# Performance work log

Hardware: AMD Instinct MI355X
Metric: run time of the kernel (lower is better)

Reference implementation:

```python
import jax, jax.numpy as jnp
import numpy as np

N = 50000   # nodes
E = 500000  # edges
NEG_SLOPE = 0.2


def _edge_softmax(e, dst, n):
    # softmax over edges grouped by destination node (DGL edge_softmax)
    m = jax.ops.segment_max(e, dst, num_segments=n)          # [N,H]
    ex = jnp.exp(e - m[dst])
    s = jax.ops.segment_sum(ex, dst, num_segments=n)
    return ex / s[dst]


def _gat(h, W, al, ar, b, src, dst, heads, d, Wres=None, act=True):
    # DGL GATConv (eval mode, no dropout)
    n = h.shape[0]
    feat = (h @ W).reshape(n, heads, d)                      # [N,H,D]
    el = jnp.sum(feat * al[None], axis=-1)                   # [N,H]
    er = jnp.sum(feat * ar[None], axis=-1)                   # [N,H]
    e = jax.nn.leaky_relu(el[src] + er[dst], NEG_SLOPE)      # [E,H]
    a = _edge_softmax(e, dst, n)                             # [E,H]
    rst = jax.ops.segment_sum(feat[src] * a[..., None], dst, num_segments=n)  # [N,H,D]
    if Wres is not None:
        res = (h @ Wres).reshape(n, heads, d)
    else:
        res = h.reshape(n, heads, d)                         # identity residual (in == heads*d)
    rst = rst + res + b.reshape(1, heads, d)
    if act:
        rst = jax.nn.elu(rst)
    return rst.reshape(n, heads * d)


def _bn(x, g, b, m, v):
    # BatchNorm1d in eval mode
    return (x - m) * g * jax.lax.rsqrt(v + 1e-5) + b


def setup_inputs() -> dict:
    key = jax.random.key(0)
    ks = jax.random.split(key, 40)
    rn = lambda i, s: jax.random.normal(ks[i], s, jnp.float32) * 0.1
    inp = dict(
        node_feats=jax.random.normal(ks[0], (N, 128), jnp.float32),
        edge_feats=jax.random.normal(ks[1], (E, 64), jnp.float32),
        src=jax.random.randint(ks[2], (E,), 0, N, jnp.int32),
        dst=jax.random.randint(ks[3], (E,), 0, N, jnp.int32),
        # GAT layer 0: 128 -> 8 heads x 16
        W0=rn(4, (128, 128)), al0=rn(5, (8, 16)), ar0=rn(6, (8, 16)), b0=rn(7, (128,)),
        g0=1.0 + rn(8, (128,)), bt0=rn(9, (128,)), m0=rn(10, (128,)),
        v0=1.0 + 0.1 * jax.random.uniform(ks[11], (128,), jnp.float32),
        # GAT layer 1: 128 -> 8 heads x 8 (residual projection)
        W1=rn(12, (128, 64)), al1=rn(13, (8, 8)), ar1=rn(14, (8, 8)), b1=rn(15, (64,)),
        Wres1=rn(16, (128, 64)),
        g1=1.0 + rn(17, (64,)), bt1=rn(18, (64,)), m1=rn(19, (64,)),
        v1=1.0 + 0.1 * jax.random.uniform(ks[20], (64,), jnp.float32),
        # GAT layer 2: 64 -> 1 head x 32 (residual projection, no activation)
        W2=rn(21, (64, 32)), al2=rn(22, (1, 32)), ar2=rn(23, (1, 32)), b2=rn(24, (32,)),
        Wres2=rn(25, (64, 32)),
        g2=1.0 + rn(26, (32,)), bt2=rn(27, (32,)), m2=rn(28, (32,)),
        v2=1.0 + 0.1 * jax.random.uniform(ks[29], (32,), jnp.float32),
        # edge projection 64 -> 128
        We=rn(30, (64, 128)), be=rn(31, (128,)),
        # edge classifier: 192 -> 32 -> 16 -> 2
        Wc1=rn(32, (192, 32)), bc1=rn(33, (32,)),
        Wc2=rn(34, (32, 16)), bc2=rn(35, (16,)),
        Wc3=rn(36, (16, 2)), bc3=rn(37, (2,)),
    )
    return inp


def reference(node_feats, edge_feats, src, dst,
              W0, al0, ar0, b0, g0, bt0, m0, v0,
              W1, al1, ar1, b1, Wres1, g1, bt1, m1, v1,
              W2, al2, ar2, b2, Wres2, g2, bt2, m2, v2,
              We, be, Wc1, bc1, Wc2, bc2, Wc3, bc3):
    h = _bn(_gat(node_feats, W0, al0, ar0, b0, src, dst, 8, 16), g0, bt0, m0, v0)
    h = _bn(_gat(h, W1, al1, ar1, b1, src, dst, 8, 8, Wres1), g1, bt1, m1, v1)
    h = _bn(_gat(h, W2, al2, ar2, b2, src, dst, 1, 32, Wres2, act=False), g2, bt2, m2, v2)
    ef = jax.nn.relu(edge_feats @ We + be)                   # [E,128]
    rep = jnp.concatenate([h[src], h[dst], ef], axis=1)      # [E,192]
    z = jax.nn.relu(rep @ Wc1 + bc1)
    z = jax.nn.relu(z @ Wc2 + bc2)
    return z @ Wc3 + bc3                                     # [E,2]
```

## Files before the change

### kernel.cpp

```cpp
#include <hip/hip_runtime.h>
#include <cfloat>
#include <math.h>

#define NEG_SLOPE 0.2f

typedef short short8 __attribute__((ext_vector_type(8)));
typedef float f32x4 __attribute__((ext_vector_type(4)));

__device__ __forceinline__ short f2bf(float x) {
    unsigned u = __float_as_uint(x);
    u += 0x7fffu + ((u >> 16) & 1u);
    return (short)(u >> 16);
}
__device__ __forceinline__ float bf2f(unsigned short s) {
    return __uint_as_float((unsigned)s << 16);
}

__device__ __forceinline__ void lds_fence() {
    __asm__ __volatile__("s_waitcnt lgkmcnt(0)" ::: "memory");
}


__global__ void count_deg_k(const int* __restrict__ dst, int* __restrict__ deg, int E) {
    int i = blockIdx.x * 256 + threadIdx.x;
    if (i < E) atomicAdd(&deg[dst[i]], 1);
}

__global__ void scanA_k(const int* __restrict__ deg, int* __restrict__ csum, int n) {
    int t = blockIdx.x * 256 + threadIdx.x;
    int ch = (n + 4095) >> 12;
    int beg = t * ch, end = min(beg + ch, n);
    int s = 0;
    for (int i = beg; i < end; ++i) s += deg[i];
    csum[t] = s;
}

__global__ void scanB_k(int* __restrict__ csum) {
    __shared__ int part[1024];
    int tid = threadIdx.x;
    int c[4];
    int s = 0;
#pragma unroll
    for (int i = 0; i < 4; ++i) { c[i] = csum[tid * 4 + i]; s += c[i]; }
    part[tid] = s;
    __syncthreads();
    for (int d = 1; d < 1024; d <<= 1) {
        int v = (tid >= d) ? part[tid - d] : 0;
        __syncthreads();
        part[tid] += v;
        __syncthreads();
    }
    int base = (tid > 0) ? part[tid - 1] : 0;
#pragma unroll
    for (int i = 0; i < 4; ++i) { csum[tid * 4 + i] = base; base += c[i]; }
}

__global__ void scanC_k(const int* __restrict__ deg, const int* __restrict__ csum,
                        int* __restrict__ off, int n, int E) {
    int t = blockIdx.x * 256 + threadIdx.x;
    int ch = (n + 4095) >> 12;
    int beg = t * ch, end = min(beg + ch, n);
    int run = csum[t];
    for (int i = beg; i < end; ++i) { off[i] = run; run += deg[i]; }
    if (t == 0) off[n] = E;
}

__global__ void scatter_k(const int* __restrict__ src, const int* __restrict__ dst,
                          const int* __restrict__ off, int* __restrict__ cur,
                          int* __restrict__ srcp, int E) {
    int i = blockIdx.x * 256 + threadIdx.x;
    if (i >= E) return;
    int d = dst[i];
    int p = off[d] + atomicAdd(&cur[d], 1);
    srcp[p] = src[i];
}


struct WSec { const float* src; short* dst; int K, OUT, base; };

__global__ void conv_w_k(const float* W0, const float* W1, const float* Wr1,
                         const float* W2, const float* Wr2, const float* Wc1,
                         const float* We, const float* Wc2,
                         short* W0T, short* W1T, short* Wr1T, short* W2T, short* Wr2T,
                         short* Wc1aT, short* Wc1bT, short* WeT, short* Wc1T, short* Wc2T) {
    int t = blockIdx.x * 256 + threadIdx.x;
    const float* src; short* dst; int K, OUT, base;
    if      (t < 16384) { src = W0;            dst = W0T;   K = 128; OUT = 128; base = 0; }
    else if (t < 24576) { src = W1;            dst = W1T;   K = 128; OUT = 64;  base = 16384; }
    else if (t < 32768) { src = Wr1;           dst = Wr1T;  K = 128; OUT = 64;  base = 24576; }
    else if (t < 34816) { src = W2;            dst = W2T;   K = 64;  OUT = 32;  base = 32768; }
    else if (t < 36864) { src = Wr2;           dst = Wr2T;  K = 64;  OUT = 32;  base = 34816; }
    else if (t < 37888) { src = Wc1;           dst = Wc1aT; K = 32;  OUT = 32;  base = 36864; }
    else if (t < 38912) { src = Wc1 + 1024;    dst = Wc1bT; K = 32;  OUT = 32;  base = 37888; }
    else if (t < 47104) { src = We;            dst = WeT;   K = 64;  OUT = 128; base = 38912; }
    else if (t < 51200) { src = Wc1 + 64 * 32; dst = Wc1T;  K = 128; OUT = 32;  base = 47104; }
    else if (t < 51712) { src = Wc2;           dst = Wc2T;  K = 32;  OUT = 16;  base = 51200; }
    else return;
    int local = t - base;
    int k = local / OUT, n = local % OUT;
    dst[n * K + k] = f2bf(src[k * OUT + n]);
}


template<int K, int NT1, int NT2, bool C1B16, bool AF32>
__global__ __launch_bounds__(256) void gemmM_k(const void* __restrict__ A,
                                               const short* __restrict__ B1T, void* __restrict__ C1,
                                               const short* __restrict__ B2T, float* __restrict__ C2,
                                               int N) {
    int w = threadIdx.x >> 6, lane = threadIdx.x & 63;
    int tile = blockIdx.x * 4 + w;
    int row0 = tile * 16;
    if (row0 >= N) return;
    int m = lane & 15, q = lane >> 4;
    int arow = row0 + m; if (arow >= N) arow = N - 1;

    constexpr int KT = K / 32;
    short8 Af[KT];
    if constexpr (AF32) {
        const float* Ap = (const float*)A + (size_t)arow * K;
#pragma unroll
        for (int kt = 0; kt < KT; ++kt) {
            float4 x = *(const float4*)&Ap[kt * 32 + q * 8];
            float4 y = *(const float4*)&Ap[kt * 32 + q * 8 + 4];
            short8 s;
            s[0] = f2bf(x.x); s[1] = f2bf(x.y); s[2] = f2bf(x.z); s[3] = f2bf(x.w);
            s[4] = f2bf(y.x); s[5] = f2bf(y.y); s[6] = f2bf(y.z); s[7] = f2bf(y.w);
            Af[kt] = s;
        }
    } else {
        const short* Ap = (const short*)A + (size_t)arow * K;
#pragma unroll
        for (int kt = 0; kt < KT; ++kt)
            Af[kt] = *(const short8*)&Ap[kt * 32 + q * 8];
    }

#pragma unroll
    for (int nt = 0; nt < NT1; ++nt) {
        f32x4 acc = {0.f, 0.f, 0.f, 0.f};
#pragma unroll
        for (int kt = 0; kt < KT; ++kt) {
            short8 b = *(const short8*)&B1T[(size_t)(nt * 16 + m) * K + kt * 32 + q * 8];
            acc = __builtin_amdgcn_mfma_f32_16x16x32_bf16(Af[kt], b, acc, 0, 0, 0);
        }
#pragma unroll
        for (int r = 0; r < 4; ++r) {
            int row = row0 + q * 4 + r;
            if (row < N) {
                if constexpr (C1B16)
                    ((short*)C1)[(size_t)row * (NT1 * 16) + nt * 16 + m] = f2bf(acc[r]);
                else
                    ((float*)C1)[(size_t)row * (NT1 * 16) + nt * 16 + m] = acc[r];
            }
        }
    }
    if constexpr (NT2 > 0) {
#pragma unroll
        for (int nt = 0; nt < NT2; ++nt) {
            f32x4 acc = {0.f, 0.f, 0.f, 0.f};
#pragma unroll
            for (int kt = 0; kt < KT; ++kt) {
                short8 b = *(const short8*)&B2T[(size_t)(nt * 16 + m) * K + kt * 32 + q * 8];
                acc = __builtin_amdgcn_mfma_f32_16x16x32_bf16(Af[kt], b, acc, 0, 0, 0);
            }
#pragma unroll
            for (int r = 0; r < 4; ++r) {
                int row = row0 + q * 4 + r;
                if (row < N)
                    C2[(size_t)row * (NT2 * 16) + nt * 16 + m] = acc[r];
            }
        }
    }
}


template<int H, int D>
__global__ void elr_k(const short* __restrict__ featb, const float* __restrict__ al,
                      const float* __restrict__ ar, float* __restrict__ el,
                      float* __restrict__ er, int n) {
    int i = blockIdx.x * 256 + threadIdx.x;
    if (i >= n * H) return;
    int h = i % H;
    const short* f = featb + (size_t)(i / H) * (H * D) + h * D;
    float sl = 0.f, sr = 0.f;
#pragma unroll
    for (int d = 0; d < D; ++d) {
        float v = bf2f((unsigned short)f[d]);
        sl = fmaf(v, al[h * D + d], sl);
        sr = fmaf(v, ar[h * D + d], sr);
    }
    el[i] = sl; er[i] = sr;
}


template<int H, int D, bool ACT>
__global__ __launch_bounds__(256) void gat_node2_k(
    const int* __restrict__ off, const int* __restrict__ srcp,
    const float* __restrict__ el, const float* __restrict__ er,
    const short* __restrict__ featb,
    const float* __restrict__ res, const float* __restrict__ bias,
    const float* __restrict__ bg, const float* __restrict__ bb,
    const float* __restrict__ bm, const float* __restrict__ bv,
    short* __restrict__ houtb, int N) {
    constexpr int HD = H * D;
    constexpr bool PAIR = (HD > 64);
    constexpr int CH = 64 / H;
    int wv_ = threadIdx.x >> 6;
    int lane = threadIdx.x & 63;
    int n = blockIdx.x * 4 + wv_;
    if (n >= N) return;
    int beg = off[n], end = off[n + 1];

    int hh = lane % H;
    int cc = lane / H;
    float ern = er[(size_t)n * H + hh];

    int k0 = PAIR ? 2 * lane : lane;
    int h0 = k0 / D; if (h0 > H - 1) h0 = H - 1;

    float acc0 = 0.f, acc1 = 0.f, svp = 0.f;

    for (int i0 = beg; i0 < end; i0 += CH) {
        int iw = i0 + cc;
        float wv = 0.f;
        int sidx = 0;
        if (iw < end) {
            sidx = srcp[iw];
            float x = el[(size_t)sidx * H + hh] + ern;
            x = x > 0.f ? x : NEG_SLOPE * x;
            wv = __expf(x);
        }
        svp += wv;
        int lim = min(end - i0, CH);
        for (int r = 0; r < lim; ++r) {
            int sl = r * H + h0;
            float w0 = __shfl(wv, sl, 64);
            int s    = __shfl(sidx, sl, 64);
            if constexpr (PAIR) {
                ushort2 uv = *(const ushort2*)&featb[(size_t)s * HD + k0];
                acc0 = fmaf(w0, bf2f(uv.x), acc0);
                acc1 = fmaf(w0, bf2f(uv.y), acc1);
            } else {
                if (lane < HD)
                    acc0 = fmaf(w0, bf2f((unsigned short)featb[(size_t)s * HD + k0]), acc0);
            }
        }
    }
#pragma unroll
    for (int mm = H; mm < 64; mm <<= 1) svp += __shfl_xor(svp, mm, 64);
    bool has_edges = end > beg;
    float inv0 = has_edges ? 1.f / __shfl(svp, h0, 64) : 0.f;

    if constexpr (PAIR) {
        float2 rs = *(const float2*)&res[(size_t)n * HD + k0];
        float2 bi = *(const float2*)&bias[k0];
        float2 gm = *(const float2*)&bm[k0];
        float2 gv = *(const float2*)&bv[k0];
        float2 gg = *(const float2*)&bg[k0];
        float2 gb = *(const float2*)&bb[k0];
        float x0 = acc0 * inv0 + rs.x + bi.x;
        float x1 = acc1 * inv0 + rs.y + bi.y;
        if (ACT) { x0 = x0 > 0.f ? x0 : expm1f(x0); x1 = x1 > 0.f ? x1 : expm1f(x1); }
        float o0 = (x0 - gm.x) * (gg.x * rsqrtf(gv.x + 1e-5f)) + gb.x;
        float o1 = (x1 - gm.y) * (gg.y * rsqrtf(gv.y + 1e-5f)) + gb.y;
        ushort2 hb;
        hb.x = (unsigned short)f2bf(o0);
        hb.y = (unsigned short)f2bf(o1);
        *(ushort2*)&houtb[(size_t)n * HD + k0] = hb;
    } else {
        if (lane < HD) {
            int k = k0;
            float x = acc0 * inv0 + res[(size_t)n * HD + k] + bias[k];
            if (ACT) x = x > 0.f ? x : expm1f(x);
            float o = (x - bm[k]) * (bg[k] * rsqrtf(bv[k] + 1e-5f)) + bb[k];
            houtb[(size_t)n * HD + k] = f2bf(o);
        }
    }
}


__global__ __launch_bounds__(256) void edge_cls_k(
    const float* __restrict__ u1, const float* __restrict__ u2,
    const float* __restrict__ edf,
    const int* __restrict__ src, const int* __restrict__ dst,
    const short* __restrict__ WeTg, const float* __restrict__ be,
    const short* __restrict__ Wc1Tg, const float* __restrict__ bc1,
    const short* __restrict__ Wc2Tg, const float* __restrict__ bc2,
    const float* __restrict__ Wc3, const float* __restrict__ bc3,
    float* __restrict__ out, int E) {
    __shared__ short efA[4][16 * 136];
    __shared__ short z1A[4][16 * 40];
    __shared__ float z2A[4][16 * 20];

    int t = threadIdx.x;
    int w = t >> 6, lane = t & 63;
    int m = lane & 15, q = lane >> 4;
    short* efW = efA[w];
    short* z1W = z1A[w];
    float* z2W = z2A[w];

    int tiles = (E + 15) >> 4;
    int gw = blockIdx.x * 4 + w;
    int W  = gridDim.x * 4;

    float beh[8];
#pragma unroll
    for (int nt = 0; nt < 8; ++nt) beh[nt] = be[nt * 16 + m];
    float bc1h0 = bc1[m], bc1h1 = bc1[16 + m];
    float bc2h = bc2[m];
    float bc30 = bc3[0], bc31 = bc3[1];

    auto ldrow = [&](int tl, float4& a, float4& b, float4& c, float4& d) {
        int em = tl * 16 + m;
        const float* rp = edf + (size_t)(em < E ? em : E - 1) * 64;
        a = *(const float4*)(rp + q * 8);
        b = *(const float4*)(rp + q * 8 + 4);
        c = *(const float4*)(rp + 32 + q * 8);
        d = *(const float4*)(rp + 32 + q * 8 + 4);
    };

    int tile = gw;
    float4 p0 = {0,0,0,0}, p1 = p0, p2 = p0, p3 = p0;
    if (tile < tiles) ldrow(tile, p0, p1, p2, p3);

    for (; tile < tiles; tile += W) {
        float4 c0 = p0, c1 = p1, c2 = p2, c3 = p3;
        int tn = tile + W;
        if (tn < tiles) ldrow(tn, p0, p1, p2, p3);

        int e0w = tile * 16;

        float u1g[2][4], u2g[2][4];
#pragma unroll
        for (int r = 0; r < 4; ++r) {
            int e = e0w + q * 4 + r;
            int ec = e < E ? e : E - 1;
            int s = src[ec], d = dst[ec];
            u1g[0][r] = u1[(size_t)s * 32 + m];
            u1g[1][r] = u1[(size_t)s * 32 + 16 + m];
            u2g[0][r] = u2[(size_t)d * 32 + m];
            u2g[1][r] = u2[(size_t)d * 32 + 16 + m];
        }

        short8 A0, A1;
        A0[0] = f2bf(c0.x); A0[1] = f2bf(c0.y); A0[2] = f2bf(c0.z); A0[3] = f2bf(c0.w);
        A0[4] = f2bf(c1.x); A0[5] = f2bf(c1.y); A0[6] = f2bf(c1.z); A0[7] = f2bf(c1.w);
        A1[0] = f2bf(c2.x); A1[1] = f2bf(c2.y); A1[2] = f2bf(c2.z); A1[3] = f2bf(c2.w);
        A1[4] = f2bf(c3.x); A1[5] = f2bf(c3.y); A1[6] = f2bf(c3.z); A1[7] = f2bf(c3.w);

#pragma unroll
        for (int nt = 0; nt < 8; ++nt) {
            int col = nt * 16 + m;
            float bias = beh[nt];
            f32x4 acc = {bias, bias, bias, bias};
            short8 b0 = *(const short8*)&WeTg[col * 64 + q * 8];
            short8 b1 = *(const short8*)&WeTg[col * 64 + 32 + q * 8];
            acc = __builtin_amdgcn_mfma_f32_16x16x32_bf16(A0, b0, acc, 0, 0, 0);
            acc = __builtin_amdgcn_mfma_f32_16x16x32_bf16(A1, b1, acc, 0, 0, 0);
#pragma unroll
            for (int r = 0; r < 4; ++r)
                efW[(q * 4 + r) * 136 + col] = f2bf(fmaxf(acc[r], 0.f));
        }
        lds_fence();

        short8 Az[4];
#pragma unroll
        for (int kt = 0; kt < 4; ++kt)
            Az[kt] = *(const short8*)&efW[m * 136 + kt * 32 + q * 8];
#pragma unroll
        for (int nt = 0; nt < 2; ++nt) {
            int col = nt * 16 + m;
            float bias = nt ? bc1h1 : bc1h0;
            f32x4 acc = {bias, bias, bias, bias};
#pragma unroll
            for (int kt = 0; kt < 4; ++kt) {
                short8 b = *(const short8*)&Wc1Tg[col * 128 + kt * 32 + q * 8];
                acc = __builtin_amdgcn_mfma_f32_16x16x32_bf16(Az[kt], b, acc, 0, 0, 0);
            }
#pragma unroll
            for (int r = 0; r < 4; ++r) {
                float z = acc[r] + u1g[nt][r] + u2g[nt][r];
                z1W[(q * 4 + r) * 40 + col] = f2bf(fmaxf(z, 0.f));
            }
        }
        lds_fence();

        {
            short8 Az1 = *(const short8*)&z1W[m * 40 + q * 8];
            short8 Bz  = *(const short8*)&Wc2Tg[m * 32 + q * 8];
            f32x4 acc = {bc2h, bc2h, bc2h, bc2h};
            acc = __builtin_amdgcn_mfma_f32_16x16x32_bf16(Az1, Bz, acc, 0, 0, 0);
#pragma unroll
            for (int r = 0; r < 4; ++r)
                z2W[(q * 4 + r) * 20 + m] = fmaxf(acc[r], 0.f);
        }
        lds_fence();

        if (lane < 16) {
            int e = lane;
            int eg = e0w + e;
            if (eg < E) {
                float a0 = bc30, a1 = bc31;
#pragma unroll
                for (int k = 0; k < 16; ++k) {
                    float z = z2W[e * 20 + k];
                    a0 = fmaf(z, Wc3[k * 2], a0);
                    a1 = fmaf(z, Wc3[k * 2 + 1], a1);
                }
                float2 o = {a0, a1};
                *(float2*)&out[(size_t)eg * 2] = o;
            }
        }
        lds_fence();
    }
}


extern "C" void kernel_launch(void* const* d_in, const int* in_sizes, int n_in,
                              void* d_out, int out_size, void* d_ws, size_t ws_size,
                              hipStream_t stream) {
    const float* node_feats = (const float*)d_in[0];
    const float* edge_feats = (const float*)d_in[1];
    const int*   src  = (const int*)d_in[2];
    const int*   dst  = (const int*)d_in[3];
    const float* W0   = (const float*)d_in[4];
    const float* al0  = (const float*)d_in[5];
    const float* ar0  = (const float*)d_in[6];
    const float* b0   = (const float*)d_in[7];
    const float* g0   = (const float*)d_in[8];
    const float* bt0  = (const float*)d_in[9];
    const float* m0   = (const float*)d_in[10];
    const float* v0   = (const float*)d_in[11];
    const float* W1   = (const float*)d_in[12];
    const float* al1  = (const float*)d_in[13];
    const float* ar1  = (const float*)d_in[14];
    const float* b1   = (const float*)d_in[15];
    const float* Wr1  = (const float*)d_in[16];
    const float* g1   = (const float*)d_in[17];
    const float* bt1  = (const float*)d_in[18];
    const float* m1   = (const float*)d_in[19];
    const float* v1   = (const float*)d_in[20];
    const float* W2   = (const float*)d_in[21];
    const float* al2  = (const float*)d_in[22];
    const float* ar2  = (const float*)d_in[23];
    const float* b2   = (const float*)d_in[24];
    const float* Wr2  = (const float*)d_in[25];
    const float* g2   = (const float*)d_in[26];
    const float* bt2  = (const float*)d_in[27];
    const float* v2m  = (const float*)d_in[28];
    const float* v2v  = (const float*)d_in[29];
    const float* We   = (const float*)d_in[30];
    const float* be   = (const float*)d_in[31];
    const float* Wc1  = (const float*)d_in[32];
    const float* bc1  = (const float*)d_in[33];
    const float* Wc2  = (const float*)d_in[34];
    const float* bc2  = (const float*)d_in[35];
    const float* Wc3  = (const float*)d_in[36];
    const float* bc3  = (const float*)d_in[37];
    float* out = (float*)d_out;

    const int N = in_sizes[0] / 128;
    const int E = in_sizes[2];

    char* p = (char*)d_ws;
    auto alloc = [&](size_t bytes) -> void* {
        void* r = (void*)p;
        p += (bytes + 255) & ~(size_t)255;
        return r;
    };
    int*   deg   = (int*)alloc((size_t)N * 4);
    int*   cur   = (int*)alloc((size_t)N * 4);
    int*   off   = (int*)alloc((size_t)(N + 1) * 4);
    int*   srcp  = (int*)alloc((size_t)E * 4);
    int*   csum  = (int*)alloc(4096 * 4);
    short* featb = (short*)alloc((size_t)N * 128 * 2);
    short* h1b   = (short*)alloc((size_t)N * 128 * 2);
    short* h2b   = (short*)alloc((size_t)N * 64 * 2);
    short* h3b   = (short*)alloc((size_t)N * 32 * 2);
    float* resf  = (float*)alloc((size_t)N * 64 * 4);
    float* u1    = (float*)alloc((size_t)N * 32 * 4);
    float* u2    = (float*)alloc((size_t)N * 32 * 4);
    float* el    = (float*)alloc((size_t)N * 8 * 4);
    float* er    = (float*)alloc((size_t)N * 8 * 4);
    short* W0T   = (short*)alloc(128 * 128 * 2);
    short* W1T   = (short*)alloc(64 * 128 * 2);
    short* Wr1T  = (short*)alloc(64 * 128 * 2);
    short* W2T   = (short*)alloc(32 * 64 * 2);
    short* Wr2T  = (short*)alloc(32 * 64 * 2);
    short* Wc1aT = (short*)alloc(32 * 32 * 2);
    short* Wc1bT = (short*)alloc(32 * 32 * 2);
    short* WeTg  = (short*)alloc(128 * 64 * 2);
    short* Wc1Tg = (short*)alloc(32 * 128 * 2);
    short* Wc2Tg = (short*)alloc(16 * 32 * 2);

    hipMemsetAsync(deg, 0, (size_t)N * 4, stream);
    hipMemsetAsync(cur, 0, (size_t)N * 4, stream);

    int eb = (E + 255) / 256;
    count_deg_k<<<eb, 256, 0, stream>>>(dst, deg, E);
    scanA_k<<<16, 256, 0, stream>>>(deg, csum, N);
    scanB_k<<<1, 1024, 0, stream>>>(csum);
    scanC_k<<<16, 256, 0, stream>>>(deg, csum, off, N, E);
    scatter_k<<<eb, 256, 0, stream>>>(src, dst, off, cur, srcp, E);
    conv_w_k<<<202, 256, 0, stream>>>(W0, W1, Wr1, W2, Wr2, Wc1, We, Wc2,
                                      W0T, W1T, Wr1T, W2T, Wr2T,
                                      Wc1aT, Wc1bT, WeTg, Wc1Tg, Wc2Tg);

    int nb4 = (N + 3) / 4;
    int gtb = ((N + 15) / 16 + 3) / 4;

    gemmM_k<128, 8, 0, true, true><<<gtb, 256, 0, stream>>>(node_feats, W0T, featb, nullptr, nullptr, N);
    elr_k<8, 16><<<(N * 8 + 255) / 256, 256, 0, stream>>>(featb, al0, ar0, el, er, N);
    gat_node2_k<8, 16, true><<<nb4, 256, 0, stream>>>(off, srcp, el, er, featb, node_feats,
                                                      b0, g0, bt0, m0, v0, h1b, N);
    gemmM_k<128, 4, 4, true, false><<<gtb, 256, 0, stream>>>(h1b, W1T, featb, Wr1T, resf, N);
    elr_k<8, 8><<<(N * 8 + 255) / 256, 256, 0, stream>>>(featb, al1, ar1, el, er, N);
    gat_node2_k<8, 8, true><<<nb4, 256, 0, stream>>>(off, srcp, el, er, featb, resf,
                                                     b1, g1, bt1, m1, v1, h2b, N);
    gemmM_k<64, 2, 2, true, false><<<gtb, 256, 0, stream>>>(h2b, W2T, featb, Wr2T, resf, N);
    elr_k<1, 32><<<(N + 255) / 256, 256, 0, stream>>>(featb, al2, ar2, el, er, N);
    gat_node2_k<1, 32, false><<<nb4, 256, 0, stream>>>(off, srcp, el, er, featb, resf,
                                                       b2, g2, bt2, v2m, v2v, h3b, N);
    gemmM_k<32, 2, 2, false, false><<<gtb, 256, 0, stream>>>(h3b, Wc1aT, u1, Wc1bT, u2, N);
    edge_cls_k<<<1024, 256, 0, stream>>>(u1, u2, edge_feats, src, dst,
                                         WeTg, be, Wc1Tg, bc1,
                                         Wc2Tg, bc2, Wc3, bc3, out, E);
}
```

Measured before the change: 577.6 us.

## Split edge classifier into an early edge-feature GEMM and a late gather MLP

```diff
diff --git a/kernel.cpp b/kernel.cpp
--- a/kernel.cpp
+++ b/kernel.cpp
@@ -5,6 +5,7 @@
 #define NEG_SLOPE 0.2f
 
 typedef short short8 __attribute__((ext_vector_type(8)));
+typedef short short4v __attribute__((ext_vector_type(4)));
 typedef float f32x4 __attribute__((ext_vector_type(4)));
 
 __device__ __forceinline__ short f2bf(float x) {
@@ -75,8 +76,6 @@
     srcp[p] = src[i];
 }
 
-
-struct WSec { const float* src; short* dst; int K, OUT, base; };
 
 __global__ void conv_w_k(const float* W0, const float* W1, const float* Wr1,
                          const float* W2, const float* Wr2, const float* Wc1,
@@ -193,7 +192,7 @@
 
 
 template<int H, int D, bool ACT>
-__global__ __launch_bounds__(256) void gat_node2_k(
+__global__ __launch_bounds__(256) void gat_node3_k(
     const int* __restrict__ off, const int* __restrict__ srcp,
     const float* __restrict__ el, const float* __restrict__ er,
     const short* __restrict__ featb,
@@ -204,6 +203,7 @@
     constexpr int HD = H * D;
     constexpr bool PAIR = (HD > 64);
     constexpr int CH = 64 / H;
+    constexpr int SB = (CH < 8) ? CH : 8;
     int wv_ = threadIdx.x >> 6;
     int lane = threadIdx.x & 63;
     int n = blockIdx.x * 4 + wv_;
@@ -231,17 +231,36 @@
         }
         svp += wv;
         int lim = min(end - i0, CH);
-        for (int r = 0; r < lim; ++r) {
-            int sl = r * H + h0;
-            float w0 = __shfl(wv, sl, 64);
-            int s    = __shfl(sidx, sl, 64);
+        for (int rb = 0; rb < lim; rb += SB) {
+            int bs = lim - rb; if (bs > SB) bs = SB;
+            float ws[SB]; int ss[SB];
+#pragma unroll
+            for (int j = 0; j < SB; ++j) {
+                int sl = (rb + j) * H + h0;
+                ws[j] = __shfl(wv, sl, 64);
+                ss[j] = __shfl(sidx, sl, 64);
+            }
             if constexpr (PAIR) {
-                ushort2 uv = *(const ushort2*)&featb[(size_t)s * HD + k0];
-                acc0 = fmaf(w0, bf2f(uv.x), acc0);
-                acc1 = fmaf(w0, bf2f(uv.y), acc1);
+                unsigned rows[SB];
+#pragma unroll
+                for (int j = 0; j < SB; ++j)
+                    if (j < bs) rows[j] = *(const unsigned*)&featb[(size_t)ss[j] * HD + k0];
+#pragma unroll
+                for (int j = 0; j < SB; ++j)
+                    if (j < bs) {
+                        acc0 = fmaf(ws[j], bf2f((unsigned short)(rows[j] & 0xffffu)), acc0);
+                        acc1 = fmaf(ws[j], bf2f((unsigned short)(rows[j] >> 16)), acc1);
+                    }
             } else {
-                if (lane < HD)
-                    acc0 = fmaf(w0, bf2f((unsigned short)featb[(size_t)s * HD + k0]), acc0);
+                unsigned short rows[SB];
+#pragma unroll
+                for (int j = 0; j < SB; ++j)
+                    if (j < bs && lane < HD)
+                        rows[j] = (unsigned short)featb[(size_t)ss[j] * HD + k0];
+#pragma unroll
+                for (int j = 0; j < SB; ++j)
+                    if (j < bs && lane < HD)
+                        acc0 = fmaf(ws[j], bf2f(rows[j]), acc0);
             }
         }
     }
@@ -278,25 +297,17 @@
 }
 
 
-__global__ __launch_bounds__(256) void edge_cls_k(
-    const float* __restrict__ u1, const float* __restrict__ u2,
+__global__ __launch_bounds__(256) void edge_t1_k(
     const float* __restrict__ edf,
-    const int* __restrict__ src, const int* __restrict__ dst,
     const short* __restrict__ WeTg, const float* __restrict__ be,
     const short* __restrict__ Wc1Tg, const float* __restrict__ bc1,
-    const short* __restrict__ Wc2Tg, const float* __restrict__ bc2,
-    const float* __restrict__ Wc3, const float* __restrict__ bc3,
-    float* __restrict__ out, int E) {
+    short* __restrict__ t1b, int E) {
     __shared__ short efA[4][16 * 136];
-    __shared__ short z1A[4][16 * 40];
-    __shared__ float z2A[4][16 * 20];
 
     int t = threadIdx.x;
     int w = t >> 6, lane = t & 63;
     int m = lane & 15, q = lane >> 4;
     short* efW = efA[w];
-    short* z1W = z1A[w];
-    float* z2W = z2A[w];
 
     int tiles = (E + 15) >> 4;
     int gw = blockIdx.x * 4 + w;
@@ -306,8 +317,6 @@
 #pragma unroll
     for (int nt = 0; nt < 8; ++nt) beh[nt] = be[nt * 16 + m];
     float bc1h0 = bc1[m], bc1h1 = bc1[16 + m];
-    float bc2h = bc2[m];
-    float bc30 = bc3[0], bc31 = bc3[1];
 
     auto ldrow = [&](int tl, float4& a, float4& b, float4& c, float4& d) {
         int em = tl * 16 + m;
@@ -329,18 +338,6 @@
 
         int e0w = tile * 16;
 
-        float u1g[2][4], u2g[2][4];
-#pragma unroll
-        for (int r = 0; r < 4; ++r) {
-            int e = e0w + q * 4 + r;
-            int ec = e < E ? e : E - 1;
-            int s = src[ec], d = dst[ec];
-            u1g[0][r] = u1[(size_t)s * 32 + m];
-            u1g[1][r] = u1[(size_t)s * 32 + 16 + m];
-            u2g[0][r] = u2[(size_t)d * 32 + m];
-            u2g[1][r] = u2[(size_t)d * 32 + 16 + m];
-        }
-
         short8 A0, A1;
         A0[0] = f2bf(c0.x); A0[1] = f2bf(c0.y); A0[2] = f2bf(c0.z); A0[3] = f2bf(c0.w);
         A0[4] = f2bf(c1.x); A0[5] = f2bf(c1.y); A0[6] = f2bf(c1.z); A0[7] = f2bf(c1.w);
@@ -378,39 +375,80 @@
             }
 #pragma unroll
             for (int r = 0; r < 4; ++r) {
-                float z = acc[r] + u1g[nt][r] + u2g[nt][r];
-                z1W[(q * 4 + r) * 40 + col] = f2bf(fmaxf(z, 0.f));
+                int e = e0w + q * 4 + r;
+                if (e < E)
+                    t1b[(size_t)e * 32 + col] = f2bf(acc[r]);
             }
         }
         lds_fence();
-
-        {
-            short8 Az1 = *(const short8*)&z1W[m * 40 + q * 8];
-            short8 Bz  = *(const short8*)&Wc2Tg[m * 32 + q * 8];
-            f32x4 acc = {bc2h, bc2h, bc2h, bc2h};
-            acc = __builtin_amdgcn_mfma_f32_16x16x32_bf16(Az1, Bz, acc, 0, 0, 0);
-#pragma unroll
-            for (int r = 0; r < 4; ++r)
-                z2W[(q * 4 + r) * 20 + m] = fmaxf(acc[r], 0.f);
-        }
-        lds_fence();
-
-        if (lane < 16) {
-            int e = lane;
-            int eg = e0w + e;
-            if (eg < E) {
-                float a0 = bc30, a1 = bc31;
-#pragma unroll
-                for (int k = 0; k < 16; ++k) {
-                    float z = z2W[e * 20 + k];
-                    a0 = fmaf(z, Wc3[k * 2], a0);
-                    a1 = fmaf(z, Wc3[k * 2 + 1], a1);
-                }
-                float2 o = {a0, a1};
-                *(float2*)&out[(size_t)eg * 2] = o;
-            }
-        }
-        lds_fence();
+    }
+}
+
+
+__global__ __launch_bounds__(256) void edge_mlp_k(
+    const short* __restrict__ t1b,
+    const float* __restrict__ u1, const float* __restrict__ u2,
+    const int* __restrict__ src, const int* __restrict__ dst,
+    const float* __restrict__ Wc2, const float* __restrict__ bc2,
+    const float* __restrict__ Wc3, const float* __restrict__ bc3,
+    float* __restrict__ out, int E) {
+    int t = threadIdx.x;
+    int w = t >> 6, lane = t & 63;
+    int g = lane >> 3;
+    int c8 = lane & 7;
+
+    float wc2r[4][16];
+#pragma unroll
+    for (int i = 0; i < 4; ++i)
+#pragma unroll
+        for (int j4 = 0; j4 < 4; ++j4)
+            *(float4*)&wc2r[i][j4 * 4] = *(const float4*)&Wc2[(c8 * 4 + i) * 16 + j4 * 4];
+
+    float bc30 = bc3[0], bc31 = bc3[1];
+
+    int base = (blockIdx.x * 4 + w) * 8;
+    int step = gridDim.x * 4 * 8;
+
+    for (int e0 = base; e0 < E; e0 += step) {
+        int e = e0 + g;
+        int ec = e < E ? e : E - 1;
+        int s = src[ec], d = dst[ec];
+        float4 u1v = *(const float4*)&u1[(size_t)s * 32 + c8 * 4];
+        float4 u2v = *(const float4*)&u2[(size_t)d * 32 + c8 * 4];
+        short4v t1v = *(const short4v*)&t1b[(size_t)ec * 32 + c8 * 4];
+
+        float z1[4];
+        z1[0] = fmaxf(bf2f((unsigned short)t1v[0]) + u1v.x + u2v.x, 0.f);
+        z1[1] = fmaxf(bf2f((unsigned short)t1v[1]) + u1v.y + u2v.y, 0.f);
+        z1[2] = fmaxf(bf2f((unsigned short)t1v[2]) + u1v.z + u2v.z, 0.f);
+        z1[3] = fmaxf(bf2f((unsigned short)t1v[3]) + u1v.w + u2v.w, 0.f);
+
+        float z2p[16];
+#pragma unroll
+        for (int j = 0; j < 16; ++j) z2p[j] = 0.f;
+#pragma unroll
+        for (int i = 0; i < 4; ++i)
+#pragma unroll
+            for (int j = 0; j < 16; ++j)
+                z2p[j] = fmaf(z1[i], wc2r[i][j], z2p[j]);
+
+#pragma unroll
+        for (int dd = 1; dd < 8; dd <<= 1)
+#pragma unroll
+            for (int j = 0; j < 16; ++j)
+                z2p[j] += __shfl_xor(z2p[j], dd, 64);
+
+        float a0 = bc30, a1 = bc31;
+#pragma unroll
+        for (int j = 0; j < 16; ++j) {
+            float z = fmaxf(z2p[j] + bc2[j], 0.f);
+            a0 = fmaf(z, Wc3[j * 2], a0);
+            a1 = fmaf(z, Wc3[j * 2 + 1], a1);
+        }
+        if (c8 == 0 && e < E) {
+            float2 o = {a0, a1};
+            *(float2*)&out[(size_t)e * 2] = o;
+        }
     }
 }
 
@@ -481,6 +519,7 @@
     float* u2    = (float*)alloc((size_t)N * 32 * 4);
     float* el    = (float*)alloc((size_t)N * 8 * 4);
     float* er    = (float*)alloc((size_t)N * 8 * 4);
+    short* t1b   = (short*)alloc((size_t)E * 32 * 2);
     short* W0T   = (short*)alloc(128 * 128 * 2);
     short* W1T   = (short*)alloc(64 * 128 * 2);
     short* Wr1T  = (short*)alloc(64 * 128 * 2);
@@ -505,23 +544,23 @@
                                       W0T, W1T, Wr1T, W2T, Wr2T,
                                       Wc1aT, Wc1bT, WeTg, Wc1Tg, Wc2Tg);
 
+    edge_t1_k<<<2048, 256, 0, stream>>>(edge_feats, WeTg, be, Wc1Tg, bc1, t1b, E);
+
     int nb4 = (N + 3) / 4;
     int gtb = ((N + 15) / 16 + 3) / 4;
 
     gemmM_k<128, 8, 0, true, true><<<gtb, 256, 0, stream>>>(node_feats, W0T, featb, nullptr, nullptr, N);
     elr_k<8, 16><<<(N * 8 + 255) / 256, 256, 0, stream>>>(featb, al0, ar0, el, er, N);
-    gat_node2_k<8, 16, true><<<nb4, 256, 0, stream>>>(off, srcp, el, er, featb, node_feats,
+    gat_node3_k<8, 16, true><<<nb4, 256, 0, stream>>>(off, srcp, el, er, featb, node_feats,
                                                       b0, g0, bt0, m0, v0, h1b, N);
     gemmM_k<128, 4, 4, true, false><<<gtb, 256, 0, stream>>>(h1b, W1T, featb, Wr1T, resf, N);
     elr_k<8, 8><<<(N * 8 + 255) / 256, 256, 0, stream>>>(featb, al1, ar1, el, er, N);
-    gat_node2_k<8, 8, true><<<nb4, 256, 0, stream>>>(off, srcp, el, er, featb, resf,
+    gat_node3_k<8, 8, true><<<nb4, 256, 0, stream>>>(off, srcp, el, er, featb, resf,
                                                      b1, g1, bt1, m1, v1, h2b, N);
     gemmM_k<64, 2, 2, true, false><<<gtb, 256, 0, stream>>>(h2b, W2T, featb, Wr2T, resf, N);
     elr_k<1, 32><<<(N + 255) / 256, 256, 0, stream>>>(featb, al2, ar2, el, er, N);
-    gat_node2_k<1, 32, false><<<nb4, 256, 0, stream>>>(off, srcp, el, er, featb, resf,
+    gat_node3_k<1, 32, false><<<nb4, 256, 0, stream>>>(off, srcp, el, er, featb, resf,
                                                        b2, g2, bt2, v2m, v2v, h3b, N);
     gemmM_k<32, 2, 2, false, false><<<gtb, 256, 0, stream>>>(h3b, Wc1aT, u1, Wc1bT, u2, N);
-    edge_cls_k<<<1024, 256, 0, stream>>>(u1, u2, edge_feats, src, dst,
-                                         WeTg, be, Wc1Tg, bc1,
-                                         Wc2Tg, bc2, Wc3, bc3, out, E);
-}
+    edge_mlp_k<<<2048, 256, 0, stream>>>(t1b, u1, u2, src, dst, Wc2, bc2, Wc3, bc3, out, E);
+}
```

Result: slower. 604.6 us (+4.7%).
